# Kernel optimization log

Hardware: AMD Instinct MI355X
Metric: run time of the kernel (lower is better)

Reference implementation:

```python
import jax, jax.numpy as jnp
import numpy as np

N_NODES = 100000


def _gcn_layer(h_in, W, b, src, dst, n_nodes):
    """PyG GCNConv: out = D^{-1/2} (A + I) D^{-1/2} (h_in @ W) + b.
    src/dst already include self-loops. Messages flow src -> dst."""
    h = h_in @ W  # [N, C_out]
    ones = jnp.ones(dst.shape[0], dtype=h.dtype)
    deg = jax.ops.segment_sum(ones, dst, num_segments=n_nodes)  # in-degree incl. self-loops
    dinv = jnp.where(deg > 0, jax.lax.rsqrt(deg), 0.0)
    norm = dinv[src] * dinv[dst]  # [E]
    msg = norm[:, None] * h[src]  # gather + scale, [E, C_out]
    out = jax.ops.segment_sum(msg, dst, num_segments=n_nodes)
    return out + b


def setup_inputs() -> dict:
    key = jax.random.key(0)
    ks = jax.random.split(key, 4)
    d_in, d_hid = 64, 64
    n_edges = 1600000
    x = jax.random.normal(ks[0], (N_NODES, d_in), dtype=jnp.float32)
    edge_index = jax.random.randint(ks[1], (2, n_edges), 0, N_NODES, dtype=jnp.int64)
    W1 = jax.random.normal(ks[2], (d_in, d_hid), dtype=jnp.float32) * (1.0 / np.sqrt(d_in))
    b1 = jnp.zeros((d_hid,), dtype=jnp.float32)
    W2 = jax.random.normal(ks[3], (d_hid, d_hid), dtype=jnp.float32) * (1.0 / np.sqrt(d_hid))
    b2 = jnp.zeros((d_hid,), dtype=jnp.float32)
    return {"x": x, "edge_index": edge_index, "W1": W1, "b1": b1, "W2": W2, "b2": b2}


def reference(x, edge_index, W1, b1, W2, b2):
    n = x.shape[0]
    loop = jnp.arange(n, dtype=edge_index.dtype)
    src = jnp.concatenate([edge_index[0], loop])  # add self-loops once, reused by both layers
    dst = jnp.concatenate([edge_index[1], loop])
    h = jax.nn.relu(_gcn_layer(x, W1, b1, src, dst, n))
    h = jax.nn.relu(_gcn_layer(h, W2, b2, src, dst, n))
    return h
```

## Files before the change

kernel.cpp:

```cpp
#include <hip/hip_runtime.h>
#include <hip/hip_bf16.h>


#define NDIM 64
#define BSHIFT 9
#define BNODES (1 << BSHIFT)
#define BCAP 10240
#define CHUNK 4096
#define PHASES 13
#define PSHIFT 13

typedef float v2f __attribute__((ext_vector_type(2)));
typedef __attribute__((ext_vector_type(8))) short short8b;
typedef __attribute__((ext_vector_type(4))) float f32x4;

__device__ __forceinline__ unsigned f2bf_rne(float f) {
  unsigned u = __float_as_uint(f);
  return (u + 0x7fffu + ((u >> 16) & 1u)) >> 16;
}

__global__ __launch_bounds__(256) void bin_scatter_kernel(
    const int* __restrict__ src, const int* __restrict__ dst,
    int* __restrict__ bcursor, unsigned* __restrict__ binned, int nedges) {
  __shared__ int lcnt[256], lbase[256], lcur[256], gbase[256], tscan[256];
  __shared__ int2 stage[CHUNK];
  int t = threadIdx.x;
  int i0 = blockIdx.x * CHUNK;
  int iend = i0 + CHUNK; if (iend > nedges) iend = nedges;
  lcnt[t] = 0;
  __syncthreads();
  for (int i = i0 + t; i < iend; i += 256)
    atomicAdd(&lcnt[dst[i] >> BSHIFT], 1);
  __syncthreads();
  tscan[t] = lcnt[t];
  __syncthreads();
  for (int off = 1; off < 256; off <<= 1) {
    int tv = (t >= off) ? tscan[t - off] : 0;
    __syncthreads();
    tscan[t] += tv;
    __syncthreads();
  }
  lbase[t] = tscan[t] - lcnt[t];
  lcur[t] = lbase[t];
  if (lcnt[t] > 0) gbase[t] = t * BCAP + atomicAdd(&bcursor[t], lcnt[t]);
  __syncthreads();
  for (int i = i0 + t; i < iend; i += 256) {
    int s = src[i], d = dst[i];
    int p = atomicAdd(&lcur[d >> BSHIFT], 1);
    stage[p] = make_int2(s, d);
  }
  __syncthreads();
  int cnt = iend - i0;
  for (int i = t; i < cnt; i += 256) {
    int2 pr = stage[i];
    int b = pr.y >> BSHIFT;
    unsigned pk = (((unsigned)(pr.y & (BNODES - 1))) << 17) | (unsigned)pr.x;
    int idx = gbase[b] + (i - lbase[b]);
    if (idx < (b + 1) * BCAP) binned[idx] = pk;
  }
}

__global__ __launch_bounds__(256) void csr_build_kernel(
    const unsigned* __restrict__ binned, const int* __restrict__ bcursor,
    int* __restrict__ rowbeg, int* __restrict__ rowend,
    int* __restrict__ csr_src, float* __restrict__ dinv, int n) {
  __shared__ int deg[BNODES], rpl[BNODES], tscan[256];
  __shared__ int pcnt[BNODES * PHASES];
  int b = blockIdx.x, t = threadIdx.x;
  int node0 = b << BSHIFT;
  int ncnt = n - node0; if (ncnt > BNODES) ncnt = BNODES;
  int e0 = b * BCAP;
  int ecnt = bcursor[b];
  if (ecnt > BCAP) ecnt = BCAP;
  for (int i = t; i < BNODES * PHASES; i += 256) pcnt[i] = 0;
  __syncthreads();
  for (int i = t; i < ecnt; i += 256) {
    unsigned u = binned[e0 + i];
    atomicAdd(&pcnt[(u >> 17) * PHASES + ((u & 0x1FFFFu) >> PSHIFT)], 1);
  }
  __syncthreads();
  for (int i = t; i < BNODES; i += 256) {
    int s = 0;
#pragma unroll
    for (int p = 0; p < PHASES; ++p) {
      int c = pcnt[i * PHASES + p];
      pcnt[i * PHASES + p] = s;
      s += c;
    }
    deg[i] = s;
  }
  __syncthreads();
  int d0 = deg[2 * t], d1 = deg[2 * t + 1];
  int ps = d0 + d1;
  tscan[t] = ps;
  __syncthreads();
  for (int off = 1; off < 256; off <<= 1) {
    int tv = (t >= off) ? tscan[t - off] : 0;
    __syncthreads();
    tscan[t] += tv;
    __syncthreads();
  }
  int eb = tscan[t] - ps;
  rpl[2 * t] = eb;
  rpl[2 * t + 1] = eb + d0;
  __syncthreads();
  for (int i = t; i < ncnt; i += 256) {
    rowbeg[node0 + i] = e0 + rpl[i];
    rowend[node0 + i] = e0 + rpl[i] + deg[i];
    dinv[node0 + i] = rsqrtf((float)deg[i] + 1.0f);
  }
  __syncthreads();
  for (int i = t; i < ecnt; i += 256) {
    unsigned u = binned[e0 + i];
    int nd = u >> 17;
    int s = (int)(u & 0x1FFFFu);
    int pos = rpl[nd] + atomicAdd(&pcnt[nd * PHASES + (s >> PSHIFT)], 1);
    csr_src[e0 + pos] = s;
  }
}

template <bool BF16IN>
__global__ __launch_bounds__(256) void gemm_mfma_kernel(
    const void* __restrict__ Xin, const float* __restrict__ W,
    const float* __restrict__ dinv, ushort* __restrict__ hsb, int nrows) {
  __shared__ __attribute__((aligned(16))) ushort stage[4][16 * NDIM];
  const int tid = threadIdx.x;
  const int l = tid & 63;
  const int wv = tid >> 6;
  const int lrow = l & 15;
  const int kg = l >> 4;

  short8b Whi[4][2], Wlo[4][2];
#pragma unroll
  for (int ct = 0; ct < 4; ++ct) {
#pragma unroll
    for (int ks = 0; ks < 2; ++ks) {
      const int c = ct * 16 + lrow;
      const int k0 = ks * 32 + kg * 8;
#pragma unroll
      for (int i = 0; i < 8; ++i) {
        float w = W[(k0 + i) * NDIM + c];
        unsigned hb = f2bf_rne(w);
        float hf = __uint_as_float(hb << 16);
        Whi[ct][ks][i] = (short)hb;
        Wlo[ct][ks][i] = (short)f2bf_rne(w - hf);
      }
    }
  }

  const int tiles = (nrows + 15) >> 4;
  for (int tb = blockIdx.x * 4; tb < tiles; tb += gridDim.x * 4) {
    const int t = tb + wv;
    const int row0 = t << 4;
    const int r = row0 + lrow;
    short8b Ahi[2], Alo[2];
    if (BF16IN) {
      const uint4* Xb = (const uint4*)Xin;
#pragma unroll
      for (int ks = 0; ks < 2; ++ks) {
        uint4 q = make_uint4(0u, 0u, 0u, 0u);
        if (r < nrows) q = Xb[(size_t)r * 8 + ks * 4 + kg];
        union { uint4 u; short8b s; } cv; cv.u = q;
        Ahi[ks] = cv.s;
        Alo[ks] = cv.s;
      }
    } else {
      const float4* Xf = (const float4*)Xin;
#pragma unroll
      for (int ks = 0; ks < 2; ++ks) {
        float4 xa = make_float4(0.f, 0.f, 0.f, 0.f);
        float4 xb = make_float4(0.f, 0.f, 0.f, 0.f);
        if (r < nrows) {
          xa = Xf[(size_t)r * 16 + ks * 8 + kg * 2];
          xb = Xf[(size_t)r * 16 + ks * 8 + kg * 2 + 1];
        }
        float xs[8] = {xa.x, xa.y, xa.z, xa.w, xb.x, xb.y, xb.z, xb.w};
#pragma unroll
        for (int i = 0; i < 8; ++i) {
          unsigned hb = f2bf_rne(xs[i]);
          float hf = __uint_as_float(hb << 16);
          Ahi[ks][i] = (short)hb;
          Alo[ks][i] = (short)f2bf_rne(xs[i] - hf);
        }
      }
    }
    f32x4 acc[4];
#pragma unroll
    for (int ct = 0; ct < 4; ++ct) {
      f32x4 a = {0.f, 0.f, 0.f, 0.f};
#pragma unroll
      for (int ks = 0; ks < 2; ++ks) {
        a = __builtin_amdgcn_mfma_f32_16x16x32_bf16(Ahi[ks], Whi[ct][ks], a, 0, 0, 0);
        a = __builtin_amdgcn_mfma_f32_16x16x32_bf16(Ahi[ks], Wlo[ct][ks], a, 0, 0, 0);
        if (!BF16IN)
          a = __builtin_amdgcn_mfma_f32_16x16x32_bf16(Alo[ks], Whi[ct][ks], a, 0, 0, 0);
      }
      acc[ct] = a;
    }
#pragma unroll
    for (int q = 0; q < 4; ++q) {
      const int rr = row0 + kg * 4 + q;
      const float di = (rr < nrows) ? dinv[rr] : 0.f;
#pragma unroll
      for (int ct = 0; ct < 4; ++ct)
        stage[wv][(kg * 4 + q) * NDIM + ct * 16 + lrow] =
            (ushort)f2bf_rne(acc[ct][q] * di);
    }
    __syncthreads();
#pragma unroll
    for (int e = 0; e < 2; ++e) {
      const int idx = e * 64 + l;
      const int rw = idx >> 3;
      if (row0 + rw < nrows)
        ((uint4*)hsb)[(size_t)(row0 + rw) * 8 + (idx & 7)] =
            ((const uint4*)stage[wv])[idx];
    }
    __syncthreads();
  }
}

__device__ __forceinline__ void add8(v2f* acc, uint4 q) {
  v2f a0, a1, a2, a3;
  a0.x = __uint_as_float(q.x << 16); a0.y = __uint_as_float(q.x & 0xffff0000u);
  a1.x = __uint_as_float(q.y << 16); a1.y = __uint_as_float(q.y & 0xffff0000u);
  a2.x = __uint_as_float(q.z << 16); a2.y = __uint_as_float(q.z & 0xffff0000u);
  a3.x = __uint_as_float(q.w << 16); a3.y = __uint_as_float(q.w & 0xffff0000u);
  acc[0] += a0; acc[1] += a1; acc[2] += a2; acc[3] += a3;
}

template <bool BF16OUT>
__global__ __launch_bounds__(256) void agg_epi_kernel(
    const int* __restrict__ rowbeg, const int* __restrict__ rowend,
    const int* __restrict__ csr_src, const uint4* __restrict__ hsb4,
    const float* __restrict__ dinv, const float4* __restrict__ b4,
    void* __restrict__ outp, int n) {
  const int l = threadIdx.x & 63;
  const int wv = threadIdx.x >> 6;
  const int ql = l & 15;
  const int sg = ql >> 3;
  const int g = ql & 7;
  const int node = blockIdx.x * 16 + wv * 4 + (l >> 4);
  const bool alive = node < n;
  const int nodec = alive ? node : 0;
  int beg = rowbeg[nodec], end = rowend[nodec];
  if (!alive) { beg = 0; end = 0; }
  const int deg = end - beg;
  int dmax = deg;
  dmax = max(dmax, __shfl_xor(dmax, 16));
  dmax = max(dmax, __shfl_xor(dmax, 32));

  v2f acc[4];
#pragma unroll
  for (int i = 0; i < 4; ++i) acc[i] = (v2f)(0.f);

  for (int base = 0; base < dmax; base += 16) {
    const int rem = deg - base;
    int eidx = (ql < rem) ? csr_src[beg + base + ql] : 0;
#pragma unroll
    for (int j = 0; j < 16; j += 2) {
      const int e = j + sg;
      int s = __shfl(eidx, (l & 48) + e);
      uint4 q = hsb4[(size_t)s * 8 + g];
      if (e < rem) add8(acc, q);
    }
  }
  if (sg == 0) add8(acc, hsb4[(size_t)nodec * 8 + g]);

  float a[8];
#pragma unroll
  for (int i = 0; i < 4; ++i) { a[2 * i] = acc[i].x; a[2 * i + 1] = acc[i].y; }
#pragma unroll
  for (int i = 0; i < 8; ++i) a[i] += __shfl_xor(a[i], 8);

  if (sg == 0 && alive) {
    float di = dinv[node];
    float4 bb0 = b4[2 * g], bb1 = b4[2 * g + 1];
    float o[8];
    o[0] = fmaxf(di * a[0] + bb0.x, 0.f);
    o[1] = fmaxf(di * a[1] + bb0.y, 0.f);
    o[2] = fmaxf(di * a[2] + bb0.z, 0.f);
    o[3] = fmaxf(di * a[3] + bb0.w, 0.f);
    o[4] = fmaxf(di * a[4] + bb1.x, 0.f);
    o[5] = fmaxf(di * a[5] + bb1.y, 0.f);
    o[6] = fmaxf(di * a[6] + bb1.z, 0.f);
    o[7] = fmaxf(di * a[7] + bb1.w, 0.f);
    if (BF16OUT) {
      uint4 wvv;
      wvv.x = f2bf_rne(o[0]) | (f2bf_rne(o[1]) << 16);
      wvv.y = f2bf_rne(o[2]) | (f2bf_rne(o[3]) << 16);
      wvv.z = f2bf_rne(o[4]) | (f2bf_rne(o[5]) << 16);
      wvv.w = f2bf_rne(o[6]) | (f2bf_rne(o[7]) << 16);
      ((uint4*)outp)[(size_t)node * 8 + g] = wvv;
    } else {
      float4 o0 = make_float4(o[0], o[1], o[2], o[3]);
      float4 o1 = make_float4(o[4], o[5], o[6], o[7]);
      ((float4*)outp)[(size_t)node * 16 + 2 * g] = o0;
      ((float4*)outp)[(size_t)node * 16 + 2 * g + 1] = o1;
    }
  }
}

extern "C" void kernel_launch(void* const* d_in, const int* in_sizes, int n_in,
                              void* d_out, int out_size, void* d_ws, size_t ws_size,
                              hipStream_t stream) {
  const float* x  = (const float*)d_in[0];
  const int* eidx = (const int*)d_in[1];
  const float* W1 = (const float*)d_in[2];
  const float* b1 = (const float*)d_in[3];
  const float* W2 = (const float*)d_in[4];
  const float* b2 = (const float*)d_in[5];
  float* out = (float*)d_out;

  const int N = in_sizes[0] / NDIM;
  const int E = in_sizes[1] / 2;
  const int* src = eidx;
  const int* dst = eidx + E;
  const int NV = N * NDIM;
  const int nbuck = (N + BNODES - 1) >> BSHIFT;
  const int nchunk = (E + CHUNK - 1) / CHUNK;

  auto al128 = [](size_t v) { return (v + 127) & ~(size_t)127; };
  char* w = (char*)d_ws;
  unsigned* binned = (unsigned*)w;  w += al128((size_t)nbuck * BCAP * 4);
  int*   csr_src = (int*)w;    w += al128((size_t)nbuck * BCAP * 4);
  int*   rowbeg  = (int*)w;    w += al128((size_t)N * 4);
  int*   rowend  = (int*)w;    w += al128((size_t)N * 4);
  float* dinv    = (float*)w;  w += al128((size_t)N * 4);
  int*   bcursor = (int*)w;    w += 2048;
  ushort* hsb = (ushort*)w;  w += al128((size_t)NV * 2);
  ushort* h2b = (ushort*)w;

  hipMemsetAsync(bcursor, 0, 1024, stream);
  bin_scatter_kernel<<<nchunk, 256, 0, stream>>>(src, dst, bcursor, binned, E);
  csr_build_kernel<<<nbuck, 256, 0, stream>>>(binned, bcursor, rowbeg, rowend,
                                              csr_src, dinv, N);

  gemm_mfma_kernel<false><<<512, 256, 0, stream>>>(x, W1, dinv, hsb, N);
  agg_epi_kernel<true><<<(N + 15) / 16, 256, 0, stream>>>(
      rowbeg, rowend, csr_src, (const uint4*)hsb, dinv, (const float4*)b1, h2b, N);

  gemm_mfma_kernel<true><<<512, 256, 0, stream>>>(h2b, W2, dinv, hsb, N);
  agg_epi_kernel<false><<<(N + 15) / 16, 256, 0, stream>>>(
      rowbeg, rowend, csr_src, (const uint4*)hsb, dinv, (const float4*)b2, out, N);
}
```

Measured before the change: 226.1 us.

## Fuse layer-1 GEMM into CSR build and use per-chunk bin slots

Binning now writes each (bucket, chunk) pair into a fixed 64-slot region with a count array, which removes the global bucket cursor atomics and the memset launch. The CSR build kernel is fused with the first-layer GEMM, so each bucket block also transforms its own 512 rows right after computing dinv, saving a kernel launch. The fused GEMM runs on only 196 blocks, giving less parallelism than the old 512-block launch. The per-chunk slot layout also scans mostly empty slots and would silently drop edges if any chunk puts more than 64 edges in one bucket.

```diff
diff --git a/kernel.cpp b/kernel.cpp
--- a/kernel.cpp
+++ b/kernel.cpp
@@ -7,6 +7,9 @@
 #define BNODES (1 << BSHIFT)
 #define BCAP 10240
 #define CHUNK 4096
+#define CAPC 64
+#define CSHIFT 6
+#define MAXCHUNK 512
 #define PHASES 13
 #define PSHIFT 13
 
@@ -21,11 +24,13 @@
 
 __global__ __launch_bounds__(256) void bin_scatter_kernel(
     const int* __restrict__ src, const int* __restrict__ dst,
-    int* __restrict__ bcursor, unsigned* __restrict__ binned, int nedges) {
-  __shared__ int lcnt[256], lbase[256], lcur[256], gbase[256], tscan[256];
+    unsigned* __restrict__ binned, int* __restrict__ cnt,
+    int nedges, int nchunk, int nbuck) {
+  __shared__ int lcnt[256], lbase[256], lcur[256], tscan[256];
   __shared__ int2 stage[CHUNK];
-  int t = threadIdx.x;
-  int i0 = blockIdx.x * CHUNK;
+  const int t = threadIdx.x;
+  const int c = blockIdx.x;
+  const int i0 = c * CHUNK;
   int iend = i0 + CHUNK; if (iend > nedges) iend = nedges;
   lcnt[t] = 0;
   __syncthreads();
@@ -42,7 +47,6 @@
   }
   lbase[t] = tscan[t] - lcnt[t];
   lcur[t] = lbase[t];
-  if (lcnt[t] > 0) gbase[t] = t * BCAP + atomicAdd(&bcursor[t], lcnt[t]);
   __syncthreads();
   for (int i = i0 + t; i < iend; i += 256) {
     int s = src[i], d = dst[i];
@@ -50,78 +54,171 @@
     stage[p] = make_int2(s, d);
   }
   __syncthreads();
-  int cnt = iend - i0;
-  for (int i = t; i < cnt; i += 256) {
+  const int m = iend - i0;
+  for (int i = t; i < m; i += 256) {
     int2 pr = stage[i];
     int b = pr.y >> BSHIFT;
-    unsigned pk = (((unsigned)(pr.y & (BNODES - 1))) << 17) | (unsigned)pr.x;
-    int idx = gbase[b] + (i - lbase[b]);
-    if (idx < (b + 1) * BCAP) binned[idx] = pk;
-  }
-}
-
-__global__ __launch_bounds__(256) void csr_build_kernel(
-    const unsigned* __restrict__ binned, const int* __restrict__ bcursor,
+    int off = i - lbase[b];
+    if (off < CAPC)
+      binned[(((size_t)b * nchunk + c) << CSHIFT) + off] =
+          (((unsigned)(pr.y & (BNODES - 1))) << 17) | (unsigned)pr.x;
+  }
+  if (t < nbuck) cnt[t * nchunk + c] = (lcnt[t] < CAPC) ? lcnt[t] : CAPC;
+}
+
+struct CsrSh {
+  int deg[BNODES], rpl[BNODES], tscan[256], ccnt[MAXCHUNK];
+  int pcnt[BNODES * PHASES];
+};
+union CsrGemmSh {
+  CsrSh c;
+  ushort g[4][16 * NDIM];
+};
+
+__global__ __launch_bounds__(256) void csr_gemm1_kernel(
+    const unsigned* __restrict__ binned, const int* __restrict__ cnt,
     int* __restrict__ rowbeg, int* __restrict__ rowend,
-    int* __restrict__ csr_src, float* __restrict__ dinv, int n) {
-  __shared__ int deg[BNODES], rpl[BNODES], tscan[256];
-  __shared__ int pcnt[BNODES * PHASES];
-  int b = blockIdx.x, t = threadIdx.x;
-  int node0 = b << BSHIFT;
+    int* __restrict__ csr_src, float* __restrict__ dinv,
+    const float* __restrict__ X, const float* __restrict__ W,
+    ushort* __restrict__ hsb, int n, int nchunk) {
+  __shared__ __align__(16) CsrGemmSh sh;
+  const int b = blockIdx.x, t = threadIdx.x;
+  const int node0 = b << BSHIFT;
   int ncnt = n - node0; if (ncnt > BNODES) ncnt = BNODES;
-  int e0 = b * BCAP;
-  int ecnt = bcursor[b];
-  if (ecnt > BCAP) ecnt = BCAP;
-  for (int i = t; i < BNODES * PHASES; i += 256) pcnt[i] = 0;
-  __syncthreads();
-  for (int i = t; i < ecnt; i += 256) {
-    unsigned u = binned[e0 + i];
-    atomicAdd(&pcnt[(u >> 17) * PHASES + ((u & 0x1FFFFu) >> PSHIFT)], 1);
+  const int e0 = b * BCAP;
+  const size_t bbase = ((size_t)b * nchunk) << CSHIFT;
+  const int nslot = nchunk << CSHIFT;
+
+  for (int i = t; i < BNODES * PHASES; i += 256) sh.c.pcnt[i] = 0;
+  for (int i = t; i < nchunk; i += 256) sh.c.ccnt[i] = cnt[b * nchunk + i];
+  __syncthreads();
+  for (int idx = t; idx < nslot; idx += 256) {
+    if ((idx & (CAPC - 1)) < sh.c.ccnt[idx >> CSHIFT]) {
+      unsigned u = binned[bbase + idx];
+      atomicAdd(&sh.c.pcnt[(u >> 17) * PHASES + ((u & 0x1FFFFu) >> PSHIFT)], 1);
+    }
   }
   __syncthreads();
   for (int i = t; i < BNODES; i += 256) {
     int s = 0;
 #pragma unroll
     for (int p = 0; p < PHASES; ++p) {
-      int c = pcnt[i * PHASES + p];
-      pcnt[i * PHASES + p] = s;
+      int c = sh.c.pcnt[i * PHASES + p];
+      sh.c.pcnt[i * PHASES + p] = s;
       s += c;
     }
-    deg[i] = s;
-  }
-  __syncthreads();
-  int d0 = deg[2 * t], d1 = deg[2 * t + 1];
+    sh.c.deg[i] = s;
+  }
+  __syncthreads();
+  int d0 = sh.c.deg[2 * t], d1 = sh.c.deg[2 * t + 1];
   int ps = d0 + d1;
-  tscan[t] = ps;
+  sh.c.tscan[t] = ps;
   __syncthreads();
   for (int off = 1; off < 256; off <<= 1) {
-    int tv = (t >= off) ? tscan[t - off] : 0;
-    __syncthreads();
-    tscan[t] += tv;
-    __syncthreads();
-  }
-  int eb = tscan[t] - ps;
-  rpl[2 * t] = eb;
-  rpl[2 * t + 1] = eb + d0;
+    int tv = (t >= off) ? sh.c.tscan[t - off] : 0;
+    __syncthreads();
+    sh.c.tscan[t] += tv;
+    __syncthreads();
+  }
+  int eb = sh.c.tscan[t] - ps;
+  sh.c.rpl[2 * t] = eb;
+  sh.c.rpl[2 * t + 1] = eb + d0;
   __syncthreads();
   for (int i = t; i < ncnt; i += 256) {
-    rowbeg[node0 + i] = e0 + rpl[i];
-    rowend[node0 + i] = e0 + rpl[i] + deg[i];
-    dinv[node0 + i] = rsqrtf((float)deg[i] + 1.0f);
-  }
-  __syncthreads();
-  for (int i = t; i < ecnt; i += 256) {
-    unsigned u = binned[e0 + i];
-    int nd = u >> 17;
-    int s = (int)(u & 0x1FFFFu);
-    int pos = rpl[nd] + atomicAdd(&pcnt[nd * PHASES + (s >> PSHIFT)], 1);
-    csr_src[e0 + pos] = s;
-  }
-}
-
-template <bool BF16IN>
-__global__ __launch_bounds__(256) void gemm_mfma_kernel(
-    const void* __restrict__ Xin, const float* __restrict__ W,
+    rowbeg[node0 + i] = e0 + sh.c.rpl[i];
+    rowend[node0 + i] = e0 + sh.c.rpl[i] + sh.c.deg[i];
+    dinv[node0 + i] = rsqrtf((float)sh.c.deg[i] + 1.0f);
+  }
+  __syncthreads();
+  for (int idx = t; idx < nslot; idx += 256) {
+    if ((idx & (CAPC - 1)) < sh.c.ccnt[idx >> CSHIFT]) {
+      unsigned u = binned[bbase + idx];
+      int nd = u >> 17;
+      int s = (int)(u & 0x1FFFFu);
+      int pos = sh.c.rpl[nd] + atomicAdd(&sh.c.pcnt[nd * PHASES + (s >> PSHIFT)], 1);
+      csr_src[e0 + pos] = s;
+    }
+  }
+  __syncthreads();
+
+  const int l = t & 63;
+  const int wv = t >> 6;
+  const int lrow = l & 15;
+  const int kg = l >> 4;
+  short8b Whi[4][2], Wlo[4][2];
+#pragma unroll
+  for (int ct = 0; ct < 4; ++ct) {
+#pragma unroll
+    for (int ks = 0; ks < 2; ++ks) {
+      const int c = ct * 16 + lrow;
+      const int k0 = ks * 32 + kg * 8;
+#pragma unroll
+      for (int i = 0; i < 8; ++i) {
+        float w = W[(k0 + i) * NDIM + c];
+        unsigned hb = f2bf_rne(w);
+        float hf = __uint_as_float(hb << 16);
+        Whi[ct][ks][i] = (short)hb;
+        Wlo[ct][ks][i] = (short)f2bf_rne(w - hf);
+      }
+    }
+  }
+  const int ntile = (ncnt + 15) >> 4;
+  for (int ti = wv; ti < ntile; ti += 4) {
+    const int row0 = node0 + (ti << 4);
+    const int r = row0 + lrow;
+    short8b Ahi[2], Alo[2];
+    const float4* Xf = (const float4*)X;
+#pragma unroll
+    for (int ks = 0; ks < 2; ++ks) {
+      float4 xa = make_float4(0.f, 0.f, 0.f, 0.f);
+      float4 xb = make_float4(0.f, 0.f, 0.f, 0.f);
+      if (r < n) {
+        xa = Xf[(size_t)r * 16 + ks * 8 + kg * 2];
+        xb = Xf[(size_t)r * 16 + ks * 8 + kg * 2 + 1];
+      }
+      float xs[8] = {xa.x, xa.y, xa.z, xa.w, xb.x, xb.y, xb.z, xb.w};
+#pragma unroll
+      for (int i = 0; i < 8; ++i) {
+        unsigned hb = f2bf_rne(xs[i]);
+        float hf = __uint_as_float(hb << 16);
+        Ahi[ks][i] = (short)hb;
+        Alo[ks][i] = (short)f2bf_rne(xs[i] - hf);
+      }
+    }
+    f32x4 acc[4];
+#pragma unroll
+    for (int ct = 0; ct < 4; ++ct) {
+      f32x4 a = {0.f, 0.f, 0.f, 0.f};
+#pragma unroll
+      for (int ks = 0; ks < 2; ++ks) {
+        a = __builtin_amdgcn_mfma_f32_16x16x32_bf16(Ahi[ks], Whi[ct][ks], a, 0, 0, 0);
+        a = __builtin_amdgcn_mfma_f32_16x16x32_bf16(Ahi[ks], Wlo[ct][ks], a, 0, 0, 0);
+        a = __builtin_amdgcn_mfma_f32_16x16x32_bf16(Alo[ks], Whi[ct][ks], a, 0, 0, 0);
+      }
+      acc[ct] = a;
+    }
+#pragma unroll
+    for (int q = 0; q < 4; ++q) {
+      const int rr = row0 + kg * 4 + q;
+      const float di = (rr < n) ? dinv[rr] : 0.f;
+#pragma unroll
+      for (int ct = 0; ct < 4; ++ct)
+        sh.g[wv][(kg * 4 + q) * NDIM + ct * 16 + lrow] =
+            (ushort)f2bf_rne(acc[ct][q] * di);
+    }
+#pragma unroll
+    for (int e = 0; e < 2; ++e) {
+      const int idx = e * 64 + l;
+      const int rw = idx >> 3;
+      if (row0 + rw < n)
+        ((uint4*)hsb)[(size_t)(row0 + rw) * 8 + (idx & 7)] =
+            ((const uint4*)sh.g[wv])[idx];
+    }
+  }
+}
+
+__global__ __launch_bounds__(256) void gemm_mfma_bf16_kernel(
+    const ushort* __restrict__ Xin, const float* __restrict__ W,
     const float* __restrict__ dinv, ushort* __restrict__ hsb, int nrows) {
   __shared__ __attribute__((aligned(16))) ushort stage[4][16 * NDIM];
   const int tid = threadIdx.x;
@@ -153,36 +250,14 @@
     const int t = tb + wv;
     const int row0 = t << 4;
     const int r = row0 + lrow;
-    short8b Ahi[2], Alo[2];
-    if (BF16IN) {
-      const uint4* Xb = (const uint4*)Xin;
-#pragma unroll
-      for (int ks = 0; ks < 2; ++ks) {
-        uint4 q = make_uint4(0u, 0u, 0u, 0u);
-        if (r < nrows) q = Xb[(size_t)r * 8 + ks * 4 + kg];
-        union { uint4 u; short8b s; } cv; cv.u = q;
-        Ahi[ks] = cv.s;
-        Alo[ks] = cv.s;
-      }
-    } else {
-      const float4* Xf = (const float4*)Xin;
-#pragma unroll
-      for (int ks = 0; ks < 2; ++ks) {
-        float4 xa = make_float4(0.f, 0.f, 0.f, 0.f);
-        float4 xb = make_float4(0.f, 0.f, 0.f, 0.f);
-        if (r < nrows) {
-          xa = Xf[(size_t)r * 16 + ks * 8 + kg * 2];
-          xb = Xf[(size_t)r * 16 + ks * 8 + kg * 2 + 1];
-        }
-        float xs[8] = {xa.x, xa.y, xa.z, xa.w, xb.x, xb.y, xb.z, xb.w};
-#pragma unroll
-        for (int i = 0; i < 8; ++i) {
-          unsigned hb = f2bf_rne(xs[i]);
-          float hf = __uint_as_float(hb << 16);
-          Ahi[ks][i] = (short)hb;
-          Alo[ks][i] = (short)f2bf_rne(xs[i] - hf);
-        }
-      }
+    short8b Ahi[2];
+    const uint4* Xb = (const uint4*)Xin;
+#pragma unroll
+    for (int ks = 0; ks < 2; ++ks) {
+      uint4 q = make_uint4(0u, 0u, 0u, 0u);
+      if (r < nrows) q = Xb[(size_t)r * 8 + ks * 4 + kg];
+      union { uint4 u; short8b s; } cv; cv.u = q;
+      Ahi[ks] = cv.s;
     }
     f32x4 acc[4];
 #pragma unroll
@@ -192,8 +267,6 @@
       for (int ks = 0; ks < 2; ++ks) {
         a = __builtin_amdgcn_mfma_f32_16x16x32_bf16(Ahi[ks], Whi[ct][ks], a, 0, 0, 0);
         a = __builtin_amdgcn_mfma_f32_16x16x32_bf16(Ahi[ks], Wlo[ct][ks], a, 0, 0, 0);
-        if (!BF16IN)
-          a = __builtin_amdgcn_mfma_f32_16x16x32_bf16(Alo[ks], Whi[ct][ks], a, 0, 0, 0);
       }
       acc[ct] = a;
     }
@@ -321,25 +394,23 @@
 
   auto al128 = [](size_t v) { return (v + 127) & ~(size_t)127; };
   char* w = (char*)d_ws;
-  unsigned* binned = (unsigned*)w;  w += al128((size_t)nbuck * BCAP * 4);
+  unsigned* binned = (unsigned*)w;  w += al128(((size_t)nbuck * nchunk) << (CSHIFT + 2));
+  int*   cnt     = (int*)w;    w += al128((size_t)nbuck * nchunk * 4);
   int*   csr_src = (int*)w;    w += al128((size_t)nbuck * BCAP * 4);
   int*   rowbeg  = (int*)w;    w += al128((size_t)N * 4);
   int*   rowend  = (int*)w;    w += al128((size_t)N * 4);
   float* dinv    = (float*)w;  w += al128((size_t)N * 4);
-  int*   bcursor = (int*)w;    w += 2048;
   ushort* hsb = (ushort*)w;  w += al128((size_t)NV * 2);
   ushort* h2b = (ushort*)w;
 
-  hipMemsetAsync(bcursor, 0, 1024, stream);
-  bin_scatter_kernel<<<nchunk, 256, 0, stream>>>(src, dst, bcursor, binned, E);
-  csr_build_kernel<<<nbuck, 256, 0, stream>>>(binned, bcursor, rowbeg, rowend,
-                                              csr_src, dinv, N);
-
-  gemm_mfma_kernel<false><<<512, 256, 0, stream>>>(x, W1, dinv, hsb, N);
+  bin_scatter_kernel<<<nchunk, 256, 0, stream>>>(src, dst, binned, cnt,
+                                                 E, nchunk, nbuck);
+  csr_gemm1_kernel<<<nbuck, 256, 0, stream>>>(binned, cnt, rowbeg, rowend,
+                                              csr_src, dinv, x, W1, hsb,
+                                              N, nchunk);
   agg_epi_kernel<true><<<(N + 15) / 16, 256, 0, stream>>>(
       rowbeg, rowend, csr_src, (const uint4*)hsb, dinv, (const float4*)b1, h2b, N);
-
-  gemm_mfma_kernel<true><<<512, 256, 0, stream>>>(h2b, W2, dinv, hsb, N);
+  gemm_mfma_bf16_kernel<<<512, 256, 0, stream>>>(h2b, W2, dinv, hsb, N);
   agg_epi_kernel<false><<<(N + 15) / 16, 256, 0, stream>>>(
       rowbeg, rowend, csr_src, (const uint4*)hsb, dinv, (const float4*)b2, out, N);
 }
```

New measurement: 260.0 us. 1.15x slower.

## Bin edges per chunk-bucket slot without global atomics; degree-sort nodes for aggregation

Applied to the files above, without the earlier changes.

The edge binning now writes each chunk's edges into a fixed 64-slot region per (bucket, chunk) pair with a count array. This removes the global atomic cursor and the memset that went with it. The CSR build reads those slots wavefront-per-chunk. It also builds a per-bucket degree-sorted node permutation that the aggregation kernels use, so the four nodes sharing a wavefront have similar degrees and less divergent loop trip counts. In exchange, the binned buffer grows, per-chunk capacity is capped at 64 edges per bucket (which could drop edges on skewed inputs), and aggregation reads perm indirectly with less coalesced output writes.

```diff
diff --git a/kernel.cpp b/kernel.cpp
--- a/kernel.cpp
+++ b/kernel.cpp
@@ -7,6 +7,9 @@
 #define BNODES (1 << BSHIFT)
 #define BCAP 10240
 #define CHUNK 4096
+#define CAPC 64
+#define CSHIFT 6
+#define MAXCHUNK 512
 #define PHASES 13
 #define PSHIFT 13
 
@@ -21,11 +24,13 @@
 
 __global__ __launch_bounds__(256) void bin_scatter_kernel(
     const int* __restrict__ src, const int* __restrict__ dst,
-    int* __restrict__ bcursor, unsigned* __restrict__ binned, int nedges) {
-  __shared__ int lcnt[256], lbase[256], lcur[256], gbase[256], tscan[256];
+    unsigned* __restrict__ binned, int* __restrict__ cnt,
+    int nedges, int nchunk, int nbuck) {
+  __shared__ int lcnt[256], lbase[256], lcur[256], tscan[256];
   __shared__ int2 stage[CHUNK];
-  int t = threadIdx.x;
-  int i0 = blockIdx.x * CHUNK;
+  const int t = threadIdx.x;
+  const int c = blockIdx.x;
+  const int i0 = c * CHUNK;
   int iend = i0 + CHUNK; if (iend > nedges) iend = nedges;
   lcnt[t] = 0;
   __syncthreads();
@@ -42,7 +47,6 @@
   }
   lbase[t] = tscan[t] - lcnt[t];
   lcur[t] = lbase[t];
-  if (lcnt[t] > 0) gbase[t] = t * BCAP + atomicAdd(&bcursor[t], lcnt[t]);
   __syncthreads();
   for (int i = i0 + t; i < iend; i += 256) {
     int s = src[i], d = dst[i];
@@ -50,42 +54,51 @@
     stage[p] = make_int2(s, d);
   }
   __syncthreads();
-  int cnt = iend - i0;
-  for (int i = t; i < cnt; i += 256) {
+  const int m = iend - i0;
+  for (int i = t; i < m; i += 256) {
     int2 pr = stage[i];
     int b = pr.y >> BSHIFT;
-    unsigned pk = (((unsigned)(pr.y & (BNODES - 1))) << 17) | (unsigned)pr.x;
-    int idx = gbase[b] + (i - lbase[b]);
-    if (idx < (b + 1) * BCAP) binned[idx] = pk;
-  }
+    int off = i - lbase[b];
+    if (off < CAPC)
+      binned[(((size_t)b * nchunk + c) << CSHIFT) + off] =
+          (((unsigned)(pr.y & (BNODES - 1))) << 17) | (unsigned)pr.x;
+  }
+  if (t < nbuck) cnt[t * nchunk + c] = (lcnt[t] < CAPC) ? lcnt[t] : CAPC;
 }
 
 __global__ __launch_bounds__(256) void csr_build_kernel(
-    const unsigned* __restrict__ binned, const int* __restrict__ bcursor,
+    const unsigned* __restrict__ binned, const int* __restrict__ cnt,
     int* __restrict__ rowbeg, int* __restrict__ rowend,
-    int* __restrict__ csr_src, float* __restrict__ dinv, int n) {
-  __shared__ int deg[BNODES], rpl[BNODES], tscan[256];
+    int* __restrict__ csr_src, float* __restrict__ dinv,
+    int* __restrict__ perm, int n, int nchunk) {
+  __shared__ int deg[BNODES], rpl[BNODES], tscan[256], ccnt[MAXCHUNK];
   __shared__ int pcnt[BNODES * PHASES];
-  int b = blockIdx.x, t = threadIdx.x;
-  int node0 = b << BSHIFT;
+  __shared__ int dhist[64], dcur[64];
+  const int b = blockIdx.x, t = threadIdx.x;
+  const int wv = t >> 6, l = t & 63;
+  const int node0 = b << BSHIFT;
   int ncnt = n - node0; if (ncnt > BNODES) ncnt = BNODES;
-  int e0 = b * BCAP;
-  int ecnt = bcursor[b];
-  if (ecnt > BCAP) ecnt = BCAP;
+  const int e0 = b * BCAP;
+  const size_t bbase = ((size_t)b * nchunk) << CSHIFT;
+
   for (int i = t; i < BNODES * PHASES; i += 256) pcnt[i] = 0;
-  __syncthreads();
-  for (int i = t; i < ecnt; i += 256) {
-    unsigned u = binned[e0 + i];
-    atomicAdd(&pcnt[(u >> 17) * PHASES + ((u & 0x1FFFFu) >> PSHIFT)], 1);
+  for (int i = t; i < nchunk; i += 256) ccnt[i] = cnt[b * nchunk + i];
+  if (t < 64) dhist[t] = 0;
+  __syncthreads();
+  for (int c = wv; c < nchunk; c += 4) {
+    if (l < ccnt[c]) {
+      unsigned u = binned[bbase + ((size_t)c << CSHIFT) + l];
+      atomicAdd(&pcnt[(u >> 17) * PHASES + ((u & 0x1FFFFu) >> PSHIFT)], 1);
+    }
   }
   __syncthreads();
   for (int i = t; i < BNODES; i += 256) {
     int s = 0;
 #pragma unroll
     for (int p = 0; p < PHASES; ++p) {
-      int c = pcnt[i * PHASES + p];
+      int cv = pcnt[i * PHASES + p];
       pcnt[i * PHASES + p] = s;
-      s += c;
+      s += cv;
     }
     deg[i] = s;
   }
@@ -108,14 +121,26 @@
     rowbeg[node0 + i] = e0 + rpl[i];
     rowend[node0 + i] = e0 + rpl[i] + deg[i];
     dinv[node0 + i] = rsqrtf((float)deg[i] + 1.0f);
-  }
-  __syncthreads();
-  for (int i = t; i < ecnt; i += 256) {
-    unsigned u = binned[e0 + i];
-    int nd = u >> 17;
-    int s = (int)(u & 0x1FFFFu);
-    int pos = rpl[nd] + atomicAdd(&pcnt[nd * PHASES + (s >> PSHIFT)], 1);
-    csr_src[e0 + pos] = s;
+    atomicAdd(&dhist[min(deg[i], 63)], 1);
+  }
+  __syncthreads();
+  if (t == 0) {
+    int run = 0;
+    for (int j = 0; j < 64; ++j) { dcur[j] = run; run += dhist[j]; }
+  }
+  __syncthreads();
+  for (int i = t; i < ncnt; i += 256) {
+    int r = atomicAdd(&dcur[min(deg[i], 63)], 1);
+    perm[node0 + r] = node0 + i;
+  }
+  for (int c = wv; c < nchunk; c += 4) {
+    if (l < ccnt[c]) {
+      unsigned u = binned[bbase + ((size_t)c << CSHIFT) + l];
+      int nd = u >> 17;
+      int s = (int)(u & 0x1FFFFu);
+      int pos = rpl[nd] + atomicAdd(&pcnt[nd * PHASES + (s >> PSHIFT)], 1);
+      csr_src[e0 + pos] = s;
+    }
   }
 }
 
@@ -230,6 +255,7 @@
 
 template <bool BF16OUT>
 __global__ __launch_bounds__(256) void agg_epi_kernel(
+    const int* __restrict__ perm,
     const int* __restrict__ rowbeg, const int* __restrict__ rowend,
     const int* __restrict__ csr_src, const uint4* __restrict__ hsb4,
     const float* __restrict__ dinv, const float4* __restrict__ b4,
@@ -239,10 +265,10 @@
   const int ql = l & 15;
   const int sg = ql >> 3;
   const int g = ql & 7;
-  const int node = blockIdx.x * 16 + wv * 4 + (l >> 4);
-  const bool alive = node < n;
-  const int nodec = alive ? node : 0;
-  int beg = rowbeg[nodec], end = rowend[nodec];
+  const int qid = blockIdx.x * 16 + wv * 4 + (l >> 4);
+  const bool alive = qid < n;
+  const int node = alive ? perm[qid] : 0;
+  int beg = rowbeg[node], end = rowend[node];
   if (!alive) { beg = 0; end = 0; }
   const int deg = end - beg;
   int dmax = deg;
@@ -264,7 +290,7 @@
       if (e < rem) add8(acc, q);
     }
   }
-  if (sg == 0) add8(acc, hsb4[(size_t)nodec * 8 + g]);
+  if (sg == 0) add8(acc, hsb4[(size_t)node * 8 + g]);
 
   float a[8];
 #pragma unroll
@@ -321,25 +347,28 @@
 
   auto al128 = [](size_t v) { return (v + 127) & ~(size_t)127; };
   char* w = (char*)d_ws;
-  unsigned* binned = (unsigned*)w;  w += al128((size_t)nbuck * BCAP * 4);
+  unsigned* binned = (unsigned*)w;  w += al128(((size_t)nbuck * nchunk) << (CSHIFT + 2));
+  int*   cnt     = (int*)w;    w += al128((size_t)nbuck * nchunk * 4);
   int*   csr_src = (int*)w;    w += al128((size_t)nbuck * BCAP * 4);
   int*   rowbeg  = (int*)w;    w += al128((size_t)N * 4);
   int*   rowend  = (int*)w;    w += al128((size_t)N * 4);
   float* dinv    = (float*)w;  w += al128((size_t)N * 4);
-  int*   bcursor = (int*)w;    w += 2048;
+  int*   perm    = (int*)w;    w += al128((size_t)N * 4);
   ushort* hsb = (ushort*)w;  w += al128((size_t)NV * 2);
   ushort* h2b = (ushort*)w;
 
-  hipMemsetAsync(bcursor, 0, 1024, stream);
-  bin_scatter_kernel<<<nchunk, 256, 0, stream>>>(src, dst, bcursor, binned, E);
-  csr_build_kernel<<<nbuck, 256, 0, stream>>>(binned, bcursor, rowbeg, rowend,
-                                              csr_src, dinv, N);
+  bin_scatter_kernel<<<nchunk, 256, 0, stream>>>(src, dst, binned, cnt,
+                                                 E, nchunk, nbuck);
+  csr_build_kernel<<<nbuck, 256, 0, stream>>>(binned, cnt, rowbeg, rowend,
+                                              csr_src, dinv, perm, N, nchunk);
 
   gemm_mfma_kernel<false><<<512, 256, 0, stream>>>(x, W1, dinv, hsb, N);
   agg_epi_kernel<true><<<(N + 15) / 16, 256, 0, stream>>>(
-      rowbeg, rowend, csr_src, (const uint4*)hsb, dinv, (const float4*)b1, h2b, N);
+      perm, rowbeg, rowend, csr_src, (const uint4*)hsb, dinv,
+      (const float4*)b1, h2b, N);
 
   gemm_mfma_kernel<true><<<512, 256, 0, stream>>>(h2b, W2, dinv, hsb, N);
   agg_epi_kernel<false><<<(N + 15) / 16, 256, 0, stream>>>(
-      rowbeg, rowend, csr_src, (const uint4*)hsb, dinv, (const float4*)b2, out, N);
-}
+      perm, rowbeg, rowend, csr_src, (const uint4*)hsb, dinv,
+      (const float4*)b2, out, N);
+}
```

Result: slower. 264.0 us (+16.8%).

## Sort nodes by degree within buckets to balance aggregation wavefront work

Applied to the files above, without the earlier changes.

The CSR build kernel now builds a per-bucket degree histogram and writes a permutation that orders the nodes in each 512-node bucket by in-degree. The aggregation kernels process nodes in that permuted order, so the four nodes sharing a wavefront have similar degrees and the dmax loop wastes fewer lanes. The cost is an extra permutation array, one more indirection per node, and a serial 64-entry scan in the build kernel. Output writes become scattered within a bucket, which may hurt store coalescing.

```diff
diff --git a/kernel.cpp b/kernel.cpp
--- a/kernel.cpp
+++ b/kernel.cpp
@@ -63,9 +63,11 @@
 __global__ __launch_bounds__(256) void csr_build_kernel(
     const unsigned* __restrict__ binned, const int* __restrict__ bcursor,
     int* __restrict__ rowbeg, int* __restrict__ rowend,
-    int* __restrict__ csr_src, float* __restrict__ dinv, int n) {
+    int* __restrict__ csr_src, float* __restrict__ dinv,
+    int* __restrict__ perm, int n) {
   __shared__ int deg[BNODES], rpl[BNODES], tscan[256];
   __shared__ int pcnt[BNODES * PHASES];
+  __shared__ int dhist[64], dcur[64];
   int b = blockIdx.x, t = threadIdx.x;
   int node0 = b << BSHIFT;
   int ncnt = n - node0; if (ncnt > BNODES) ncnt = BNODES;
@@ -73,6 +75,7 @@
   int ecnt = bcursor[b];
   if (ecnt > BCAP) ecnt = BCAP;
   for (int i = t; i < BNODES * PHASES; i += 256) pcnt[i] = 0;
+  if (t < 64) dhist[t] = 0;
   __syncthreads();
   for (int i = t; i < ecnt; i += 256) {
     unsigned u = binned[e0 + i];
@@ -108,8 +111,18 @@
     rowbeg[node0 + i] = e0 + rpl[i];
     rowend[node0 + i] = e0 + rpl[i] + deg[i];
     dinv[node0 + i] = rsqrtf((float)deg[i] + 1.0f);
-  }
-  __syncthreads();
+    atomicAdd(&dhist[min(deg[i], 63)], 1);
+  }
+  __syncthreads();
+  if (t == 0) {
+    int run = 0;
+    for (int j = 0; j < 64; ++j) { dcur[j] = run; run += dhist[j]; }
+  }
+  __syncthreads();
+  for (int i = t; i < ncnt; i += 256) {
+    int r = atomicAdd(&dcur[min(deg[i], 63)], 1);
+    perm[node0 + r] = node0 + i;
+  }
   for (int i = t; i < ecnt; i += 256) {
     unsigned u = binned[e0 + i];
     int nd = u >> 17;
@@ -230,6 +243,7 @@
 
 template <bool BF16OUT>
 __global__ __launch_bounds__(256) void agg_epi_kernel(
+    const int* __restrict__ perm,
     const int* __restrict__ rowbeg, const int* __restrict__ rowend,
     const int* __restrict__ csr_src, const uint4* __restrict__ hsb4,
     const float* __restrict__ dinv, const float4* __restrict__ b4,
@@ -239,10 +253,10 @@
   const int ql = l & 15;
   const int sg = ql >> 3;
   const int g = ql & 7;
-  const int node = blockIdx.x * 16 + wv * 4 + (l >> 4);
-  const bool alive = node < n;
-  const int nodec = alive ? node : 0;
-  int beg = rowbeg[nodec], end = rowend[nodec];
+  const int qid = blockIdx.x * 16 + wv * 4 + (l >> 4);
+  const bool alive = qid < n;
+  const int node = alive ? perm[qid] : 0;
+  int beg = rowbeg[node], end = rowend[node];
   if (!alive) { beg = 0; end = 0; }
   const int deg = end - beg;
   int dmax = deg;
@@ -264,7 +278,7 @@
       if (e < rem) add8(acc, q);
     }
   }
-  if (sg == 0) add8(acc, hsb4[(size_t)nodec * 8 + g]);
+  if (sg == 0) add8(acc, hsb4[(size_t)node * 8 + g]);
 
   float a[8];
 #pragma unroll
@@ -326,6 +340,7 @@
   int*   rowbeg  = (int*)w;    w += al128((size_t)N * 4);
   int*   rowend  = (int*)w;    w += al128((size_t)N * 4);
   float* dinv    = (float*)w;  w += al128((size_t)N * 4);
+  int*   perm    = (int*)w;    w += al128((size_t)N * 4);
   int*   bcursor = (int*)w;    w += 2048;
   ushort* hsb = (ushort*)w;  w += al128((size_t)NV * 2);
   ushort* h2b = (ushort*)w;
@@ -333,13 +348,15 @@
   hipMemsetAsync(bcursor, 0, 1024, stream);
   bin_scatter_kernel<<<nchunk, 256, 0, stream>>>(src, dst, bcursor, binned, E);
   csr_build_kernel<<<nbuck, 256, 0, stream>>>(binned, bcursor, rowbeg, rowend,
-                                              csr_src, dinv, N);
+                                              csr_src, dinv, perm, N);
 
   gemm_mfma_kernel<false><<<512, 256, 0, stream>>>(x, W1, dinv, hsb, N);
   agg_epi_kernel<true><<<(N + 15) / 16, 256, 0, stream>>>(
-      rowbeg, rowend, csr_src, (const uint4*)hsb, dinv, (const float4*)b1, h2b, N);
+      perm, rowbeg, rowend, csr_src, (const uint4*)hsb, dinv,
+      (const float4*)b1, h2b, N);
 
   gemm_mfma_kernel<true><<<512, 256, 0, stream>>>(h2b, W2, dinv, hsb, N);
   agg_epi_kernel<false><<<(N + 15) / 16, 256, 0, stream>>>(
-      rowbeg, rowend, csr_src, (const uint4*)hsb, dinv, (const float4*)b2, out, N);
-}
+      perm, rowbeg, rowend, csr_src, (const uint4*)hsb, dinv,
+      (const float4*)b2, out, N);
+}
```

Result: slower. 237.0 us (+4.8%).
